# Performance work log

Measured on AMD Instinct MI355X. Metric: run time of the kernel, lower is better.

The kernel has to match this reference:

```python
import jax, jax.numpy as jnp
import numpy as np

B, C, HH, WW = 8, 512, 32, 32
HEADS, GROUPS, EPS = 8, 32, 1e-5


def setup_inputs() -> dict:
    key = jax.random.key(0)
    k0, k1, k2 = jax.random.split(key, 3)
    x = jax.random.normal(k0, (B, C, HH, WW), jnp.float32)
    gamma = jnp.ones((C,), jnp.float32)
    beta = jnp.zeros((C,), jnp.float32)
    # 1x1 convs modeled as (out, in) matrices; fan-in scaling keeps logits sane
    w_qkv = jax.random.normal(k1, (3 * C, C), jnp.float32) * (C ** -0.5)
    b_qkv = jnp.zeros((3 * C,), jnp.float32)
    w_proj = jax.random.normal(k2, (C, C), jnp.float32) * (C ** -0.5)
    b_proj = jnp.zeros((C,), jnp.float32)
    return {"x": x, "gamma": gamma, "beta": beta, "w_qkv": w_qkv,
            "b_qkv": b_qkv, "w_proj": w_proj, "b_proj": b_proj}


def reference(x, gamma, beta, w_qkv, b_qkv, w_proj, b_proj):
    b, c, h, w = x.shape
    S = h * w
    xr = x.reshape(b, c, S)
    # GroupNorm(32, C) over (channels_in_group, spatial)
    xg = xr.reshape(b, GROUPS, c // GROUPS, S)
    mu = xg.mean(axis=(2, 3), keepdims=True)
    var = xg.var(axis=(2, 3), keepdims=True)
    xn = ((xg - mu) * jax.lax.rsqrt(var + EPS)).reshape(b, c, S)
    xn = xn * gamma[None, :, None] + beta[None, :, None]
    # qkv 1x1 conv: (B, 3C, S)
    qkv = jnp.einsum('oc,bcs->bos', w_qkv, xn) + b_qkv[None, :, None]
    D = c // HEADS
    qkv = qkv.reshape(b, 3, HEADS, D, S)  # channel layout: (three, H, D)
    q = jnp.transpose(qkv[:, 0], (0, 1, 3, 2))  # (B, H, S, D)
    k = jnp.transpose(qkv[:, 1], (0, 1, 3, 2))
    v = jnp.transpose(qkv[:, 2], (0, 1, 3, 2))
    scale = 1.0 / float(np.sqrt(np.sqrt(D)))
    logits = jnp.einsum('bhtd,bhsd->bhts', q * scale, k * scale)  # (B,H,S,S)
    logits = logits - jnp.max(logits, axis=-1, keepdims=True)
    probs = jax.nn.softmax(logits, axis=-1)  # dropout p=0 (default)
    attn = jnp.einsum('bhts,bhsd->bhtd', probs, v)  # (B,H,S,D)
    hout = jnp.transpose(attn, (0, 1, 3, 2)).reshape(b, c, S)  # (B, H*D=C, S)
    hout = jnp.einsum('oc,bcs->bos', w_proj, hout) + b_proj[None, :, None]
    return (hout + xr).reshape(b, c, h, w)
```

## Files before the change

kernel.cpp:

```cpp
#include <hip/hip_runtime.h>
#include <hip/hip_bf16.h>

typedef __hip_bfloat16 bf16;
typedef unsigned short u16;
typedef __attribute__((ext_vector_type(8))) short bf16x8;
typedef __attribute__((ext_vector_type(4))) float f32x4;
typedef __attribute__((ext_vector_type(16))) float f32x16;

static constexpr int Bn = 8;
static constexpr int C = 512;
static constexpr int S = 1024;
static constexpr int NH = 8;
static constexpr int HD = 64;
static constexpr int CPG = 16;
#define EPSV 1e-5f
#define QSCALE 0.18033688011112042f

__device__ __forceinline__ u16 f2bf(float f) {
    bf16 h = __float2bfloat16(f);
    return *reinterpret_cast<u16*>(&h);
}
__device__ __forceinline__ unsigned pack_bf2(float a, float b) {
    __hip_bfloat162 h = __float22bfloat162_rn(make_float2(a, b));
    return *reinterpret_cast<unsigned*>(&h);
}

__device__ __forceinline__ void async_copy16(const void* g, void* l) {
    __builtin_amdgcn_global_load_lds(
        (const __attribute__((address_space(1))) void*)g,
        (__attribute__((address_space(3))) void*)l, 16, 0, 0);
}

__global__ __launch_bounds__(256) void prep(const float* __restrict__ x,
                                            const float* __restrict__ wqkv,
                                            const float* __restrict__ wproj,
                                            float* __restrict__ stats,
                                            u16* __restrict__ wbf) {
    const int tid = threadIdx.x;
    if (blockIdx.x < 256) {
        const int bg = blockIdx.x;
        const size_t base = (size_t)bg * CPG * S;
        const int N = CPG * S;
        float sum = 0.f, sq = 0.f;
        for (int i = tid * 4; i < N; i += 1024) {
            float4 v = *reinterpret_cast<const float4*>(&x[base + i]);
            sum += v.x + v.y + v.z + v.w;
            sq += v.x * v.x + v.y * v.y + v.z * v.z + v.w * v.w;
        }
#pragma unroll
        for (int off = 32; off > 0; off >>= 1) {
            sum += __shfl_down(sum, off, 64);
            sq  += __shfl_down(sq,  off, 64);
        }
        __shared__ float s0[4], s1[4];
        if ((tid & 63) == 0) { s0[tid >> 6] = sum; s1[tid >> 6] = sq; }
        __syncthreads();
        if (tid == 0) {
            float a  = s0[0] + s0[1] + s0[2] + s0[3];
            float b2 = s1[0] + s1[1] + s1[2] + s1[3];
            float mu = a / (float)N;
            float var = fmaxf(b2 / (float)N - mu * mu, 0.f);
            stats[bg] = mu;
            stats[256 + bg] = rsqrtf(var + EPSV);
        }
    } else {
        int idx = (blockIdx.x - 256) * 1024 + tid * 4;
        float4 v;
        float sc = 1.f;
        if (idx < 1536 * 512) {
            v = *reinterpret_cast<const float4*>(&wqkv[idx]);
            if (idx < 512 * 512) sc = QSCALE;
        } else {
            v = *reinterpret_cast<const float4*>(&wproj[idx - 1536 * 512]);
        }
        u16 t[4] = {f2bf(v.x * sc), f2bf(v.y * sc), f2bf(v.z * sc), f2bf(v.w * sc)};
        *reinterpret_cast<uint2*>(&wbf[idx]) = *reinterpret_cast<uint2*>(t);
    }
}

__global__ __launch_bounds__(256) void gn_apply_t(const float* __restrict__ x,
                                                  const float* __restrict__ gamma,
                                                  const float* __restrict__ beta,
                                                  const float* __restrict__ stats,
                                                  u16* __restrict__ xnt) {
    const int b = blockIdx.z, c0 = blockIdx.y * 64, s0 = blockIdx.x * 64;
    const int tid = threadIdx.x;
    __shared__ u16 T[64 * 72];
    const float* xb = x + ((size_t)b * C + c0) * S;
#pragma unroll
    for (int i = 0; i < 4; ++i) {
        int ch = i * 256 + tid;
        int c = ch >> 4, seg = ch & 15;
        int cg = c0 + c;
        float mu = stats[b * 32 + (cg >> 4)];
        float rstd = stats[256 + b * 32 + (cg >> 4)];
        float ga = gamma[cg], be = beta[cg];
        float4 v = *reinterpret_cast<const float4*>(&xb[(size_t)c * S + s0 + seg * 4]);
        float vals[4] = {v.x, v.y, v.z, v.w};
#pragma unroll
        for (int j = 0; j < 4; ++j)
            T[(seg * 4 + j) * 72 + c] = f2bf((vals[j] - mu) * rstd * ga + be);
    }
    __syncthreads();
#pragma unroll
    for (int i = 0; i < 2; ++i) {
        int ch = i * 256 + tid;
        int r = ch >> 3, seg = ch & 7;
        uint4 val = *reinterpret_cast<const uint4*>(&T[r * 72 + seg * 8]);
        *reinterpret_cast<uint4*>(&xnt[(size_t)(b * S + s0 + r) * C + c0 + seg * 8]) = val;
    }
}

template <int MODE>
__global__ __launch_bounds__(256) void mfma_gemm(const u16* __restrict__ Wb,
                                                 const u16* __restrict__ Xt,
                                                 const float* __restrict__ bias,
                                                 const float* __restrict__ resid,
                                                 u16* __restrict__ qkvT,
                                                 u16* __restrict__ qkvV,
                                                 float* __restrict__ Yf) {
    const int K = 512;
    const int b = blockIdx.z, o0 = blockIdx.y * 128, s0 = blockIdx.x * 128;
    const int tid = threadIdx.x;
    const int lane = tid & 63, w = tid >> 6;
    const int l31 = lane & 31, half = lane >> 5;
    const int wr = w >> 1, wc = w & 1;
    __shared__ u16 As[128 * 64];
    __shared__ u16 Bs[128 * 64];
    f32x16 acc[2][2] = {};
    const u16* Xb = Xt + (size_t)(b * S + s0) * K;
    for (int k0 = 0; k0 < K; k0 += 64) {
#pragma unroll
        for (int i = 0; i < 4; ++i) {
            int ci = w * 4 + i;
            int r = ci * 8 + (lane >> 3);
            int c = (lane & 7) ^ (r & 7);
            async_copy16(&Wb[(size_t)(o0 + r) * K + k0 + c * 8], &As[ci * 512]);
            async_copy16(&Xb[(size_t)r * K + k0 + c * 8], &Bs[ci * 512]);
        }
        __syncthreads();
#pragma unroll
        for (int kk = 0; kk < 4; ++kk) {
            int c8 = kk * 2 + half;
            bf16x8 af[2], bfr[2];
#pragma unroll
            for (int mt = 0; mt < 2; ++mt) {
                int R = wr * 64 + mt * 32 + l31;
                af[mt] = *reinterpret_cast<const bf16x8*>(
                    &As[R * 64 + ((c8 ^ (R & 7)) << 3)]);
            }
#pragma unroll
            for (int nt = 0; nt < 2; ++nt) {
                int R = wc * 64 + nt * 32 + l31;
                bfr[nt] = *reinterpret_cast<const bf16x8*>(
                    &Bs[R * 64 + ((c8 ^ (R & 7)) << 3)]);
            }
#pragma unroll
            for (int mt = 0; mt < 2; ++mt)
#pragma unroll
                for (int nt = 0; nt < 2; ++nt)
                    acc[mt][nt] = __builtin_amdgcn_mfma_f32_32x32x16_bf16(
                        af[mt], bfr[nt], acc[mt][nt], 0, 0, 0);
        }
        __syncthreads();
    }
    if (MODE == 1) {
#pragma unroll
        for (int mt = 0; mt < 2; ++mt) {
#pragma unroll
            for (int g = 0; g < 4; ++g) {
                int o_b = o0 + wr * 64 + mt * 32 + g * 8 + half * 4;
                float4 bz = *reinterpret_cast<const float4*>(&bias[o_b]);
                float bza[4] = {bz.x, bz.y, bz.z, bz.w};
#pragma unroll
                for (int nt = 0; nt < 2; ++nt) {
                    int s = s0 + wc * 64 + nt * 32 + l31;
#pragma unroll
                    for (int r = 0; r < 4; ++r) {
                        size_t idx = (size_t)(b * C + o_b + r) * S + s;
                        Yf[idx] = acc[mt][nt][g * 4 + r] + bza[r] + resid[idx];
                    }
                }
            }
        }
    } else if (o0 < 1024) {
        float bsc = (o0 < 512) ? QSCALE : 1.f;
#pragma unroll
        for (int mt = 0; mt < 2; ++mt) {
#pragma unroll
            for (int g = 0; g < 4; ++g) {
                int o_b = o0 + wr * 64 + mt * 32 + g * 8 + half * 4;
                float4 bz = *reinterpret_cast<const float4*>(&bias[o_b]);
#pragma unroll
                for (int nt = 0; nt < 2; ++nt) {
                    int s = s0 + wc * 64 + nt * 32 + l31;
                    uint2 pk;
                    pk.x = pack_bf2(acc[mt][nt][g * 4 + 0] + bz.x * bsc,
                                    acc[mt][nt][g * 4 + 1] + bz.y * bsc);
                    pk.y = pack_bf2(acc[mt][nt][g * 4 + 2] + bz.z * bsc,
                                    acc[mt][nt][g * 4 + 3] + bz.w * bsc);
                    *reinterpret_cast<uint2*>(&qkvT[(size_t)(b * S + s) * 1024 + o_b]) = pk;
                }
            }
        }
    } else {
#pragma unroll
        for (int mt = 0; mt < 2; ++mt) {
#pragma unroll
            for (int g = 0; g < 4; ++g) {
                int o_b = o0 - 1024 + wr * 64 + mt * 32 + g * 8 + half * 4;
                float4 bz = *reinterpret_cast<const float4*>(&bias[1024 + o_b]);
                float bza[4] = {bz.x, bz.y, bz.z, bz.w};
#pragma unroll
                for (int nt = 0; nt < 2; ++nt) {
                    int s = s0 + wc * 64 + nt * 32 + l31;
#pragma unroll
                    for (int r = 0; r < 4; ++r)
                        qkvV[(size_t)(b * 512 + o_b + r) * S + s] =
                            f2bf(acc[mt][nt][g * 4 + r] + bza[r]);
                }
            }
        }
    }
}

__global__ __launch_bounds__(256) void attn_mfma(const u16* __restrict__ qkvT,
                                                 const u16* __restrict__ qkvV,
                                                 u16* __restrict__ houtt) {
    const int b = blockIdx.x >> 3, h = blockIdx.x & 7, q0 = blockIdx.y * 128;
    const int tid = threadIdx.x;
    const int lane = tid & 63, w = tid >> 6;
    const int l31 = lane & 31, half = lane >> 5;
    __shared__ u16 ks[2][64 * 64];
    __shared__ u16 vs[2][64 * 64];
    __shared__ u16 ps[128 * 68];

    const u16* qrow = qkvT + (size_t)(b * S + q0 + w * 32 + l31) * 1024 + h * HD;
    const u16* krow = qkvT + (size_t)b * S * 1024 + 512 + h * HD;
    const u16* vrow = qkvV + (size_t)(b * 512 + h * HD) * S;

    bf16x8 qfrag[4];
#pragma unroll
    for (int kk = 0; kk < 4; ++kk)
        qfrag[kk] = *reinterpret_cast<const bf16x8*>(&qrow[kk * 16 + half * 8]);

#pragma unroll
    for (int i = 0; i < 2; ++i) {
        int ci = w * 2 + i;
        int r = ci * 8 + (lane >> 3);
        int c = (lane & 7) ^ (r & 7);
        async_copy16(&krow[(size_t)r * 1024 + c * 8], &ks[0][ci * 512]);
        async_copy16(&vrow[(size_t)r * S + c * 8], &vs[0][ci * 512]);
    }
    __syncthreads();

    f32x16 o_acc[2] = {};
    float l_i = 0.f;
    const int prow = (w * 32 + l31) * 68;

    for (int t = 0; t < 16; ++t) {
        const int cur = t & 1, nxt = cur ^ 1;
        if (t < 15) {
            int kt = (t + 1) * 64;
#pragma unroll
            for (int i = 0; i < 2; ++i) {
                int ci = w * 2 + i;
                int r = ci * 8 + (lane >> 3);
                int c = (lane & 7) ^ (r & 7);
                async_copy16(&krow[(size_t)(kt + r) * 1024 + c * 8], &ks[nxt][ci * 512]);
                async_copy16(&vrow[(size_t)r * S + kt + c * 8], &vs[nxt][ci * 512]);
            }
        }
        f32x16 s_acc[2] = {};
#pragma unroll
        for (int mt = 0; mt < 2; ++mt) {
            int r = mt * 32 + l31;
#pragma unroll
            for (int kk = 0; kk < 4; ++kk) {
                int c8 = kk * 2 + half;
                bf16x8 kf = *reinterpret_cast<const bf16x8*>(
                    &ks[cur][r * 64 + ((c8 ^ (r & 7)) << 3)]);
                s_acc[mt] = __builtin_amdgcn_mfma_f32_32x32x16_bf16(
                    kf, qfrag[kk], s_acc[mt], 0, 0, 0);
            }
        }
        float rs = 0.f;
#pragma unroll
        for (int mt = 0; mt < 2; ++mt)
#pragma unroll
            for (int g = 0; g < 4; ++g) {
                float p0 = __builtin_amdgcn_exp2f(s_acc[mt][g * 4 + 0]);
                float p1 = __builtin_amdgcn_exp2f(s_acc[mt][g * 4 + 1]);
                float p2 = __builtin_amdgcn_exp2f(s_acc[mt][g * 4 + 2]);
                float p3 = __builtin_amdgcn_exp2f(s_acc[mt][g * 4 + 3]);
                rs += (p0 + p1) + (p2 + p3);
                uint2 pk;
                pk.x = pack_bf2(p0, p1);
                pk.y = pack_bf2(p2, p3);
                *reinterpret_cast<uint2*>(&ps[prow + mt * 32 + g * 8 + half * 4]) = pk;
            }
        l_i += rs;
        bf16x8 pf[4];
#pragma unroll
        for (int kk = 0; kk < 4; ++kk) {
            union { uint2 u[2]; bf16x8 v; } u8;
            u8.u[0] = *reinterpret_cast<const uint2*>(&ps[prow + kk * 16 + half * 8]);
            u8.u[1] = *reinterpret_cast<const uint2*>(&ps[prow + kk * 16 + half * 8 + 4]);
            pf[kk] = u8.v;
        }
#pragma unroll
        for (int nt = 0; nt < 2; ++nt) {
            int rv = nt * 32 + l31;
#pragma unroll
            for (int kk = 0; kk < 4; ++kk) {
                int c8 = kk * 2 + half;
                bf16x8 vf = *reinterpret_cast<const bf16x8*>(
                    &vs[cur][rv * 64 + ((c8 ^ (rv & 7)) << 3)]);
                o_acc[nt] = __builtin_amdgcn_mfma_f32_32x32x16_bf16(
                    vf, pf[kk], o_acc[nt], 0, 0, 0);
            }
        }
        __syncthreads();
    }
    l_i += __shfl_xor(l_i, 32, 64);
    float inv = 1.f / l_i;
    u16* orow = houtt + (size_t)(b * S + q0 + w * 32 + l31) * 512 + h * HD;
#pragma unroll
    for (int nt = 0; nt < 2; ++nt)
#pragma unroll
        for (int g = 0; g < 4; ++g) {
            uint2 pk;
            pk.x = pack_bf2(o_acc[nt][g * 4 + 0] * inv, o_acc[nt][g * 4 + 1] * inv);
            pk.y = pack_bf2(o_acc[nt][g * 4 + 2] * inv, o_acc[nt][g * 4 + 3] * inv);
            *reinterpret_cast<uint2*>(&orow[nt * 32 + g * 8 + half * 4]) = pk;
        }
}

extern "C" void kernel_launch(void* const* d_in, const int* in_sizes, int n_in,
                              void* d_out, int out_size, void* d_ws, size_t ws_size,
                              hipStream_t stream) {
    const float* x      = (const float*)d_in[0];
    const float* gamma  = (const float*)d_in[1];
    const float* beta   = (const float*)d_in[2];
    const float* w_qkv  = (const float*)d_in[3];
    const float* b_qkv  = (const float*)d_in[4];
    const float* w_proj = (const float*)d_in[5];
    const float* b_proj = (const float*)d_in[6];
    float* out = (float*)d_out;

    char* ws = (char*)d_ws;
    float* stats = (float*)ws;
    u16* wbf   = (u16*)(ws + 4096);
    u16* xnt   = (u16*)(ws + 4096 + 2097152);
    u16* qkvT  = (u16*)(ws + 4096 + 2097152 + 8388608);
    u16* qkvV  = (u16*)(ws + 4096 + 2097152 + 8388608 + 16777216);
    u16* houtt = xnt;

    prep<<<1280, 256, 0, stream>>>(x, w_qkv, w_proj, stats, wbf);
    gn_apply_t<<<dim3(16, 8, Bn), 256, 0, stream>>>(x, gamma, beta, stats, xnt);
    mfma_gemm<0><<<dim3(8, 12, Bn), 256, 0, stream>>>(
        wbf, xnt, b_qkv, nullptr, qkvT, qkvV, nullptr);
    attn_mfma<<<dim3(Bn * NH, S / 128), 256, 0, stream>>>(qkvT, qkvV, houtt);
    mfma_gemm<1><<<dim3(8, 4, Bn), 256, 0, stream>>>(
        wbf + 1536 * 512, houtt, b_proj, x, nullptr, nullptr, out);
}
```

Before: 156.4 us.

## Cache bf16 copy of x for GroupNorm and residual; shrink proj GEMM tile

The stats pass now also writes a bf16 copy of x. The GroupNorm apply kernel and the projection epilogue's residual add read that copy instead of the fp32 input, cutting their global read traffic in half. The projection GEMM is split into its own kernel with 64-row output tiles, which doubles its block count to fill more CUs. The cost is one extra 8 MB write in the prep kernel. It also loses precision, because the residual x is rounded to bf16 before it is added to the output.

```diff
diff --git a/kernel.cpp b/kernel.cpp
--- a/kernel.cpp
+++ b/kernel.cpp
@@ -4,7 +4,6 @@
 typedef __hip_bfloat16 bf16;
 typedef unsigned short u16;
 typedef __attribute__((ext_vector_type(8))) short bf16x8;
-typedef __attribute__((ext_vector_type(4))) float f32x4;
 typedef __attribute__((ext_vector_type(16))) float f32x16;
 
 static constexpr int Bn = 8;
@@ -20,6 +19,10 @@
     bf16 h = __float2bfloat16(f);
     return *reinterpret_cast<u16*>(&h);
 }
+__device__ __forceinline__ float bf2f(u16 u) {
+    bf16 h = *reinterpret_cast<bf16*>(&u);
+    return __bfloat162float(h);
+}
 __device__ __forceinline__ unsigned pack_bf2(float a, float b) {
     __hip_bfloat162 h = __float22bfloat162_rn(make_float2(a, b));
     return *reinterpret_cast<unsigned*>(&h);
@@ -35,7 +38,8 @@
                                             const float* __restrict__ wqkv,
                                             const float* __restrict__ wproj,
                                             float* __restrict__ stats,
-                                            u16* __restrict__ wbf) {
+                                            u16* __restrict__ wbf,
+                                            u16* __restrict__ xb16) {
     const int tid = threadIdx.x;
     if (blockIdx.x < 256) {
         const int bg = blockIdx.x;
@@ -46,6 +50,10 @@
             float4 v = *reinterpret_cast<const float4*>(&x[base + i]);
             sum += v.x + v.y + v.z + v.w;
             sq += v.x * v.x + v.y * v.y + v.z * v.z + v.w * v.w;
+            uint2 pk;
+            pk.x = pack_bf2(v.x, v.y);
+            pk.y = pack_bf2(v.z, v.w);
+            *reinterpret_cast<uint2*>(&xb16[base + i]) = pk;
         }
 #pragma unroll
         for (int off = 32; off > 0; off >>= 1) {
@@ -78,7 +86,7 @@
     }
 }
 
-__global__ __launch_bounds__(256) void gn_apply_t(const float* __restrict__ x,
+__global__ __launch_bounds__(256) void gn_apply_t(const u16* __restrict__ xb16,
                                                   const float* __restrict__ gamma,
                                                   const float* __restrict__ beta,
                                                   const float* __restrict__ stats,
@@ -86,7 +94,7 @@
     const int b = blockIdx.z, c0 = blockIdx.y * 64, s0 = blockIdx.x * 64;
     const int tid = threadIdx.x;
     __shared__ u16 T[64 * 72];
-    const float* xb = x + ((size_t)b * C + c0) * S;
+    const u16* xb = xb16 + ((size_t)b * C + c0) * S;
 #pragma unroll
     for (int i = 0; i < 4; ++i) {
         int ch = i * 256 + tid;
@@ -95,11 +103,12 @@
         float mu = stats[b * 32 + (cg >> 4)];
         float rstd = stats[256 + b * 32 + (cg >> 4)];
         float ga = gamma[cg], be = beta[cg];
-        float4 v = *reinterpret_cast<const float4*>(&xb[(size_t)c * S + s0 + seg * 4]);
-        float vals[4] = {v.x, v.y, v.z, v.w};
+        uint2 raw = *reinterpret_cast<const uint2*>(&xb[(size_t)c * S + s0 + seg * 4]);
+        u16 r4[4];
+        *reinterpret_cast<uint2*>(r4) = raw;
 #pragma unroll
         for (int j = 0; j < 4; ++j)
-            T[(seg * 4 + j) * 72 + c] = f2bf((vals[j] - mu) * rstd * ga + be);
+            T[(seg * 4 + j) * 72 + c] = f2bf((bf2f(r4[j]) - mu) * rstd * ga + be);
     }
     __syncthreads();
 #pragma unroll
@@ -111,14 +120,11 @@
     }
 }
 
-template <int MODE>
-__global__ __launch_bounds__(256) void mfma_gemm(const u16* __restrict__ Wb,
-                                                 const u16* __restrict__ Xt,
-                                                 const float* __restrict__ bias,
-                                                 const float* __restrict__ resid,
-                                                 u16* __restrict__ qkvT,
-                                                 u16* __restrict__ qkvV,
-                                                 float* __restrict__ Yf) {
+__global__ __launch_bounds__(256) void qkv_gemm(const u16* __restrict__ Wb,
+                                                const u16* __restrict__ Xt,
+                                                const float* __restrict__ bias,
+                                                u16* __restrict__ qkvT,
+                                                u16* __restrict__ qkvV) {
     const int K = 512;
     const int b = blockIdx.z, o0 = blockIdx.y * 128, s0 = blockIdx.x * 128;
     const int tid = threadIdx.x;
@@ -164,26 +170,7 @@
         }
         __syncthreads();
     }
-    if (MODE == 1) {
-#pragma unroll
-        for (int mt = 0; mt < 2; ++mt) {
-#pragma unroll
-            for (int g = 0; g < 4; ++g) {
-                int o_b = o0 + wr * 64 + mt * 32 + g * 8 + half * 4;
-                float4 bz = *reinterpret_cast<const float4*>(&bias[o_b]);
-                float bza[4] = {bz.x, bz.y, bz.z, bz.w};
-#pragma unroll
-                for (int nt = 0; nt < 2; ++nt) {
-                    int s = s0 + wc * 64 + nt * 32 + l31;
-#pragma unroll
-                    for (int r = 0; r < 4; ++r) {
-                        size_t idx = (size_t)(b * C + o_b + r) * S + s;
-                        Yf[idx] = acc[mt][nt][g * 4 + r] + bza[r] + resid[idx];
-                    }
-                }
-            }
-        }
-    } else if (o0 < 1024) {
+    if (o0 < 1024) {
         float bsc = (o0 < 512) ? QSCALE : 1.f;
 #pragma unroll
         for (int mt = 0; mt < 2; ++mt) {
@@ -219,6 +206,71 @@
                         qkvV[(size_t)(b * 512 + o_b + r) * S + s] =
                             f2bf(acc[mt][nt][g * 4 + r] + bza[r]);
                 }
+            }
+        }
+    }
+}
+
+__global__ __launch_bounds__(256) void proj_gemm(const u16* __restrict__ Wb,
+                                                 const u16* __restrict__ Xt,
+                                                 const float* __restrict__ bias,
+                                                 const u16* __restrict__ residb,
+                                                 float* __restrict__ Yf) {
+    const int K = 512;
+    const int b = blockIdx.z, o0 = blockIdx.y * 64, s0 = blockIdx.x * 128;
+    const int tid = threadIdx.x;
+    const int lane = tid & 63, w = tid >> 6;
+    const int l31 = lane & 31, half = lane >> 5;
+    const int wr = w >> 1, wc = w & 1;
+    __shared__ u16 As[64 * 64];
+    __shared__ u16 Bs[128 * 64];
+    f32x16 acc[2] = {};
+    const u16* Xb = Xt + (size_t)(b * S + s0) * K;
+    for (int k0 = 0; k0 < K; k0 += 64) {
+#pragma unroll
+        for (int i = 0; i < 2; ++i) {
+            int ci = w * 2 + i;
+            int r = ci * 8 + (lane >> 3);
+            int c = (lane & 7) ^ (r & 7);
+            async_copy16(&Wb[(size_t)(o0 + r) * K + k0 + c * 8], &As[ci * 512]);
+        }
+#pragma unroll
+        for (int i = 0; i < 4; ++i) {
+            int ci = w * 4 + i;
+            int r = ci * 8 + (lane >> 3);
+            int c = (lane & 7) ^ (r & 7);
+            async_copy16(&Xb[(size_t)r * K + k0 + c * 8], &Bs[ci * 512]);
+        }
+        __syncthreads();
+#pragma unroll
+        for (int kk = 0; kk < 4; ++kk) {
+            int c8 = kk * 2 + half;
+            int Ra = wr * 32 + l31;
+            bf16x8 af = *reinterpret_cast<const bf16x8*>(
+                &As[Ra * 64 + ((c8 ^ (Ra & 7)) << 3)]);
+#pragma unroll
+            for (int nt = 0; nt < 2; ++nt) {
+                int R = wc * 64 + nt * 32 + l31;
+                bf16x8 bfr = *reinterpret_cast<const bf16x8*>(
+                    &Bs[R * 64 + ((c8 ^ (R & 7)) << 3)]);
+                acc[nt] = __builtin_amdgcn_mfma_f32_32x32x16_bf16(
+                    af, bfr, acc[nt], 0, 0, 0);
+            }
+        }
+        __syncthreads();
+    }
+#pragma unroll
+    for (int g = 0; g < 4; ++g) {
+        int o_b = o0 + wr * 32 + g * 8 + half * 4;
+        float4 bz = *reinterpret_cast<const float4*>(&bias[o_b]);
+        float bza[4] = {bz.x, bz.y, bz.z, bz.w};
+#pragma unroll
+        for (int nt = 0; nt < 2; ++nt) {
+            int s = s0 + wc * 64 + nt * 32 + l31;
+#pragma unroll
+            for (int r = 0; r < 4; ++r) {
+                size_t idx = (size_t)(b * C + o_b + r) * S + s;
+                Yf[idx] = acc[nt][g * 4 + r] + bza[r] + bf2f(residb[idx]);
             }
         }
     }
@@ -351,16 +403,16 @@
     char* ws = (char*)d_ws;
     float* stats = (float*)ws;
     u16* wbf   = (u16*)(ws + 4096);
-    u16* xnt   = (u16*)(ws + 4096 + 2097152);
-    u16* qkvT  = (u16*)(ws + 4096 + 2097152 + 8388608);
-    u16* qkvV  = (u16*)(ws + 4096 + 2097152 + 8388608 + 16777216);
+    u16* xb16  = (u16*)(ws + 4096 + (size_t)2097152);
+    u16* xnt   = (u16*)(ws + 4096 + (size_t)18874368);
+    u16* qkvT  = (u16*)(ws + 4096 + (size_t)27262976);
+    u16* qkvV  = (u16*)(ws + 4096 + (size_t)44040192);
     u16* houtt = xnt;
 
-    prep<<<1280, 256, 0, stream>>>(x, w_qkv, w_proj, stats, wbf);
-    gn_apply_t<<<dim3(16, 8, Bn), 256, 0, stream>>>(x, gamma, beta, stats, xnt);
-    mfma_gemm<0><<<dim3(8, 12, Bn), 256, 0, stream>>>(
-        wbf, xnt, b_qkv, nullptr, qkvT, qkvV, nullptr);
+    prep<<<1280, 256, 0, stream>>>(x, w_qkv, w_proj, stats, wbf, xb16);
+    gn_apply_t<<<dim3(16, 8, Bn), 256, 0, stream>>>(xb16, gamma, beta, stats, xnt);
+    qkv_gemm<<<dim3(8, 12, Bn), 256, 0, stream>>>(wbf, xnt, b_qkv, qkvT, qkvV);
     attn_mfma<<<dim3(Bn * NH, S / 128), 256, 0, stream>>>(qkvT, qkvV, houtt);
-    mfma_gemm<1><<<dim3(8, 4, Bn), 256, 0, stream>>>(
-        wbf + 1536 * 512, houtt, b_proj, x, nullptr, nullptr, out);
-}
+    proj_gemm<<<dim3(8, 8, Bn), 256, 0, stream>>>(
+        wbf + 1536 * 512, houtt, b_proj, xb16, out);
+}
```

Result: no change. 158.6 us (+1.4%).
